# Kernel optimization log

Measured on AMD Instinct MI355X. Metric: run time of the kernel, lower is better.

## Reference

```python
import jax, jax.numpy as jnp
import numpy as np

NUM_HEADS = 16
HEAD_DIM = 128
D_MODEL = 2048
BATCH = 2
SEQ = 2048


def setup_inputs() -> dict:
    key = jax.random.key(0)
    ks = jax.random.split(key, 6)
    x = jax.random.normal(ks[0], (BATCH, SEQ, D_MODEL), dtype=jnp.float32)
    # RoPE tables (real/imag parts of freqs_cis), shape [S, HEAD_DIM//2]
    pos = jnp.arange(SEQ, dtype=jnp.float32)[:, None]
    inv_freq = 1.0 / (10000.0 ** (jnp.arange(0, HEAD_DIM, 2, dtype=jnp.float32) / HEAD_DIM))
    ang = pos * inv_freq[None, :]
    freq_cos = jnp.cos(ang)
    freq_sin = jnp.sin(ang)
    scale = 1.0 / np.sqrt(D_MODEL)
    wq = jax.random.normal(ks[1], (D_MODEL, NUM_HEADS * HEAD_DIM), dtype=jnp.float32) * scale
    wk = jax.random.normal(ks[2], (D_MODEL, NUM_HEADS * HEAD_DIM), dtype=jnp.float32) * scale
    wv = jax.random.normal(ks[3], (D_MODEL, NUM_HEADS * HEAD_DIM), dtype=jnp.float32) * scale
    wo = jax.random.normal(ks[4], (NUM_HEADS * HEAD_DIM, D_MODEL), dtype=jnp.float32) * scale
    return {"x": x, "freq_cos": freq_cos, "freq_sin": freq_sin,
            "wq": wq, "wk": wk, "wv": wv, "wo": wo}


def _rotate_half(t):
    half = t.shape[-1] // 2
    return jnp.concatenate([-t[..., half:], t[..., :half]], axis=-1)


def _apply_rope(q, k, freq_cos, freq_sin):
    # q, k: [B, H, S, D]; freq_cos/sin: [S_total, D//2]
    q = q.astype(jnp.float32)
    k = k.astype(jnp.float32)
    S = q.shape[2]
    cos = jnp.concatenate([freq_cos[:S], freq_cos[:S]], axis=-1)[None, None]  # [1,1,S,D]
    sin = jnp.concatenate([freq_sin[:S], freq_sin[:S]], axis=-1)[None, None]
    q_out = q * cos + _rotate_half(q) * sin
    k_out = k * cos + _rotate_half(k) * sin
    return q_out, k_out


def reference(x, freq_cos, freq_sin, wq, wk, wv, wo):
    B, S, D = x.shape
    H, hd = NUM_HEADS, HEAD_DIM
    q = (x @ wq).reshape(B, S, H, hd).transpose(0, 2, 1, 3)  # [B,H,S,hd]
    k = (x @ wk).reshape(B, S, H, hd).transpose(0, 2, 1, 3)
    v = (x @ wv).reshape(B, S, H, hd).transpose(0, 2, 1, 3)
    q, k = _apply_rope(q, k, freq_cos, freq_sin)
    # explicit causal attention (faithful to CPU/GPU path)
    logits = jnp.einsum('bhqd,bhkd->bhqk', q, k) / jnp.sqrt(jnp.float32(hd))
    mask = jnp.tril(jnp.ones((S, S), dtype=jnp.float32))
    logits = jnp.where(mask[None, None, :, :], logits, -1e10)
    weights = jax.nn.softmax(logits, axis=-1)
    out = jnp.einsum('bhqk,bhkd->bhqd', weights, v)  # [B,H,S,hd]
    out = out.transpose(0, 2, 1, 3).reshape(B, S, H * hd)
    return out @ wo
```

## Files before the change

kernel.cpp:

```cpp
#include <hip/hip_runtime.h>

typedef unsigned short u16;
typedef unsigned int u32;
typedef __attribute__((ext_vector_type(8))) short bf16x8;
typedef __attribute__((ext_vector_type(4))) short bf16x4;
typedef __attribute__((ext_vector_type(4))) float f32x4;
typedef __attribute__((ext_vector_type(16))) float f32x16;

#define MFMA(a, b, c) __builtin_amdgcn_mfma_f32_16x16x32_bf16(a, b, c, 0, 0, 0)
#define MFMA32(a, b, c) __builtin_amdgcn_mfma_f32_32x32x16_bf16(a, b, c, 0, 0, 0)
#define ASYNC16(g, l)                                                        \
  __builtin_amdgcn_global_load_lds(                                          \
      (const __attribute__((address_space(1))) u32*)(g),                     \
      (__attribute__((address_space(3))) u32*)(l), 16, 0, 0)

#define SBARRIER()                                                           \
  do {                                                                       \
    asm volatile("" ::: "memory");                                           \
    __builtin_amdgcn_s_barrier();                                            \
    asm volatile("" ::: "memory");                                           \
  } while (0)

__device__ __forceinline__ float b2f(u16 u) {
  union { u32 i; float f; } x; x.i = ((u32)u) << 16; return x.f;
}
__device__ __forceinline__ u16 f2b(float f) {
  union { float f; u32 i; } x; x.f = f;
  return (u16)((x.i + 0x7fff + ((x.i >> 16) & 1)) >> 16);
}
__device__ __forceinline__ f32x4 fzero4() { f32x4 z = {0.f, 0.f, 0.f, 0.f}; return z; }
__device__ __forceinline__ f32x16 fzero16() {
  f32x16 z;
#pragma unroll
  for (int i = 0; i < 16; ++i) z[i] = 0.f;
  return z;
}
__device__ __forceinline__ u32 pkbf16(float lo, float hi) {
  u32 r;
  asm("v_cvt_pk_bf16_f32 %0, %1, %2" : "=v"(r) : "v"(lo), "v"(hi));
  return r;
}

__global__ __launch_bounds__(256) void cvt_x(const float* __restrict__ src,
                                             u16* __restrict__ dst) {
  const int i = (blockIdx.x * 256 + threadIdx.x) * 4;
  const f32x4 v = *(const f32x4*)(src + i);
  bf16x4 o;
  o[0] = (short)f2b(v[0]); o[1] = (short)f2b(v[1]);
  o[2] = (short)f2b(v[2]); o[3] = (short)f2b(v[3]);
  *(bf16x4*)(dst + i) = o;
}

__global__ __launch_bounds__(256) void wtrans_f32(const float* __restrict__ src,
                                                  u16* __restrict__ dst) {
  __shared__ u16 tile[64][65];
  const int k0 = blockIdx.y * 64, n0 = blockIdx.x * 64;
  const int t = threadIdx.x;
  const int tr = t >> 3, tc = t & 7;

#pragma unroll
  for (int hh = 0; hh < 2; ++hh) {
    const int k = tr + hh * 32;
    const float* p = src + (size_t)(k0 + k) * 2048 + n0 + tc * 8;
    const f32x4 a = *(const f32x4*)(p);
    const f32x4 b = *(const f32x4*)(p + 4);
#pragma unroll
    for (int j = 0; j < 4; ++j) tile[k][tc * 8 + j] = f2b(a[j]);
#pragma unroll
    for (int j = 0; j < 4; ++j) tile[k][tc * 8 + 4 + j] = f2b(b[j]);
  }
  __syncthreads();
#pragma unroll
  for (int hh = 0; hh < 2; ++hh) {
    const int n = tr + hh * 32;
    bf16x8 v;
#pragma unroll
    for (int j = 0; j < 8; ++j) v[j] = (short)tile[tc * 8 + j][n];
    *(bf16x8*)(dst + (size_t)(n0 + n) * 2048 + k0 + tc * 8) = v;
  }
}

__global__ __launch_bounds__(256) void wtrans3(const float* __restrict__ wq,
                                               const float* __restrict__ wk,
                                               const float* __restrict__ wv,
                                               u16* __restrict__ wTall) {
  __shared__ u16 tile[64][65];
  const int z = blockIdx.z;
  const float* src = (z == 0) ? wq : (z == 1) ? wk : wv;
  u16* dst = wTall + (size_t)z * 2048 * 2048;
  const int k0 = blockIdx.y * 64, n0 = blockIdx.x * 64;
  const int t = threadIdx.x;
  const int tr = t >> 3, tc = t & 7;

#pragma unroll
  for (int hh = 0; hh < 2; ++hh) {
    const int k = tr + hh * 32;
    const float* p = src + (size_t)(k0 + k) * 2048 + n0 + tc * 8;
    const f32x4 a = *(const f32x4*)(p);
    const f32x4 b = *(const f32x4*)(p + 4);
#pragma unroll
    for (int j = 0; j < 4; ++j) tile[k][tc * 8 + j] = f2b(a[j]);
#pragma unroll
    for (int j = 0; j < 4; ++j) tile[k][tc * 8 + 4 + j] = f2b(b[j]);
  }
  __syncthreads();
#pragma unroll
  for (int hh = 0; hh < 2; ++hh) {
    const int n = tr + hh * 32;
    bf16x8 v;
#pragma unroll
    for (int j = 0; j < 8; ++j) v[j] = (short)tile[tc * 8 + j][n];
    *(bf16x8*)(dst + (size_t)(n0 + n) * 2048 + k0 + tc * 8) = v;
  }
}

__device__ __forceinline__ void gemm_mainloop(const u16* __restrict__ A,
                                              const u16* __restrict__ Bt,
                                              int K, int m0, int n0,
                                              u16* lA, u16* lB,
                                              f32x4 acc[4][4]) {
  const int tid = threadIdx.x;
  const int lane = tid & 63;
  const int wave = tid >> 6;
  const int quad = lane >> 4;
  const int l16 = lane & 15;
  const int wr = wave >> 1, wc = wave & 1;

  const int srow = lane >> 2;
  const int scol = (lane & 3) * 8;
  const u16* ga0 = A + (size_t)(m0 + (wave * 2 + 0) * 16 + srow) * K + scol;
  const u16* ga1 = A + (size_t)(m0 + (wave * 2 + 1) * 16 + srow) * K + scol;
  const u16* gb0 = Bt + (size_t)(n0 + (wave * 2 + 0) * 16 + srow) * K + scol;
  const u16* gb1 = Bt + (size_t)(n0 + (wave * 2 + 1) * 16 + srow) * K + scol;
  u16* la0 = lA + (wave * 2 + 0) * 512;
  u16* la1 = lA + (wave * 2 + 1) * 512;
  u16* lb0 = lB + (wave * 2 + 0) * 512;
  u16* lb1 = lB + (wave * 2 + 1) * 512;

  for (int k0 = 0; k0 < K; k0 += 32) {
    ASYNC16(ga0 + k0, la0);
    ASYNC16(ga1 + k0, la1);
    ASYNC16(gb0 + k0, lb0);
    ASYNC16(gb1 + k0, lb1);
    __syncthreads();
    bf16x8 af[4], bfr[4];
#pragma unroll
    for (int mb = 0; mb < 4; ++mb)
      af[mb] = *(const bf16x8*)(lA + ((wr * 64 + mb * 16 + l16) * 32 + quad * 8));
#pragma unroll
    for (int nb = 0; nb < 4; ++nb)
      bfr[nb] = *(const bf16x8*)(lB + ((wc * 64 + nb * 16 + l16) * 32 + quad * 8));
#pragma unroll
    for (int mb = 0; mb < 4; ++mb)
#pragma unroll
      for (int nb = 0; nb < 4; ++nb)
        acc[mb][nb] = MFMA(af[mb], bfr[nb], acc[mb][nb]);
    __syncthreads();
  }
}

__global__ __launch_bounds__(256) void gemm_qkv(const u16* __restrict__ x,
                                                const u16* __restrict__ wT,
                                                u16* __restrict__ qkv) {
  __shared__ u16 lA[128 * 32];
  __shared__ u16 lB[128 * 32];
  f32x4 acc[4][4];
#pragma unroll
  for (int i = 0; i < 4; ++i)
#pragma unroll
    for (int j = 0; j < 4; ++j) acc[i][j] = fzero4();

  const int m0 = blockIdx.y * 128, n0 = blockIdx.x * 128;
  gemm_mainloop(x, wT, 2048, m0, n0, lA, lB, acc);

  const int lane = threadIdx.x & 63, wave = threadIdx.x >> 6;
  const int quad = lane >> 4, l16 = lane & 15;
  const int wr = wave >> 1, wc = wave & 1;
#pragma unroll
  for (int mb = 0; mb < 4; ++mb)
#pragma unroll
    for (int nb = 0; nb < 4; ++nb)
#pragma unroll
      for (int r = 0; r < 4; ++r) {
        const int row = m0 + wr * 64 + mb * 16 + quad * 4 + r;
        const int col = n0 + wc * 64 + nb * 16 + l16;
        const int b = row >> 11, s = row & 2047;
        const int which = col >> 11, rem = col & 2047;
        const int hh = rem >> 7, d = rem & 127;
        const size_t idx = (size_t)which * ((size_t)4096 * 2048) +
                           (((size_t)(b * 16 + hh) * 2048 + s) * 128 + d);
        qkv[idx] = f2b(acc[mb][nb][r]);
      }
}

__global__ __launch_bounds__(512, 2) void gemm_out8(const u16* __restrict__ Oin,
                                                    const u16* __restrict__ woT,
                                                    float* __restrict__ out) {
  __shared__ u16 lds[3 * 24576];

  const int orig = blockIdx.x;
  const int wg = (orig & 7) * 32 + (orig >> 3);
  const int m0 = (wg >> 4) * 256;
  const int n0 = (wg & 15) * 128;

  const int tid = threadIdx.x;
  const int lane = tid & 63;
  const int wave = tid >> 6;
  const int quad = lane >> 4, l16 = lane & 15;
  const int wr = wave >> 2, wc = wave & 3;

  const int r0s = tid >> 3;
  const int c0s = (tid & 7) ^ (r0s & 7);
  const int r1s = r0s + 64;
  const int c1s = (tid & 7) ^ (r1s & 7);

  const u16* gA = Oin + (size_t)m0 * 2048;
  const u16* gB = woT + (size_t)n0 * 2048;

#define SLOT8(t) (lds + ((t) % 3) * 24576)
#define STAGE_A8(t)                                                          \
  do {                                                                       \
    u16* Lb0 = SLOT8(t) + wave * 512;                                        \
    const u16* g0 = gA + (t) * 64;                                           \
    ASYNC16(g0 + (size_t)r0s * 2048 + c0s * 8, Lb0);                         \
    ASYNC16(g0 + (size_t)r1s * 2048 + c1s * 8, Lb0 + 4096);                  \
    u16* Lb1 = SLOT8(t) + 8192 + wave * 512;                                 \
    const u16* g1 = gA + (size_t)128 * 2048 + (t) * 64;                      \
    ASYNC16(g1 + (size_t)r0s * 2048 + c0s * 8, Lb1);                         \
    ASYNC16(g1 + (size_t)r1s * 2048 + c1s * 8, Lb1 + 4096);                  \
  } while (0)
#define STAGE_B8(t)                                                          \
  do {                                                                       \
    u16* Lb = SLOT8(t) + 16384 + wave * 512;                                 \
    const u16* g = gB + (t) * 64;                                            \
    ASYNC16(g + (size_t)r0s * 2048 + c0s * 8, Lb);                           \
    ASYNC16(g + (size_t)r1s * 2048 + c1s * 8, Lb + 4096);                    \
  } while (0)

  f32x4 acc[8][2];
#pragma unroll
  for (int i = 0; i < 8; ++i) { acc[i][0] = fzero4(); acc[i][1] = fzero4(); }

  int aoff[8], boff[2];
#pragma unroll
  for (int mb = 0; mb < 8; ++mb) aoff[mb] = (wr * 128 + mb * 16 + l16) * 64;
#pragma unroll
  for (int nb = 0; nb < 2; ++nb) boff[nb] = 16384 + (wc * 32 + nb * 16 + l16) * 64;
  const int ach0 = ((0 * 4 + quad) ^ (l16 & 7)) * 8;
  const int ach1 = ((1 * 4 + quad) ^ (l16 & 7)) * 8;

  STAGE_A8(0); STAGE_B8(0);
  STAGE_A8(1); STAGE_B8(1);
  asm volatile("s_waitcnt vmcnt(6)" ::: "memory");
  SBARRIER();

  for (int t = 0; t < 32; ++t) {
    const u16* sl = SLOT8(t);
    bf16x8 af[8], bfr[2];

#pragma unroll
    for (int mb = 0; mb < 8; ++mb)
      af[mb] = *(const bf16x8*)(sl + aoff[mb] + ach0);
#pragma unroll
    for (int nb = 0; nb < 2; ++nb)
      bfr[nb] = *(const bf16x8*)(sl + boff[nb] + ach0);
    if (t < 30) STAGE_A8(t + 2);
    SBARRIER();
    asm volatile("s_waitcnt lgkmcnt(0)" ::: "memory");
    __builtin_amdgcn_s_setprio(1);
#pragma unroll
    for (int mb = 0; mb < 8; ++mb)
#pragma unroll
      for (int nb = 0; nb < 2; ++nb)
        acc[mb][nb] = MFMA(af[mb], bfr[nb], acc[mb][nb]);
    __builtin_amdgcn_s_setprio(0);
    SBARRIER();

#pragma unroll
    for (int mb = 0; mb < 8; ++mb)
      af[mb] = *(const bf16x8*)(sl + aoff[mb] + ach1);
#pragma unroll
    for (int nb = 0; nb < 2; ++nb)
      bfr[nb] = *(const bf16x8*)(sl + boff[nb] + ach1);
    if (t < 30) STAGE_B8(t + 2);
    SBARRIER();
    asm volatile("s_waitcnt lgkmcnt(0)" ::: "memory");
    __builtin_amdgcn_s_setprio(1);
#pragma unroll
    for (int mb = 0; mb < 8; ++mb)
#pragma unroll
      for (int nb = 0; nb < 2; ++nb)
        acc[mb][nb] = MFMA(af[mb], bfr[nb], acc[mb][nb]);
    __builtin_amdgcn_s_setprio(0);
    if (t <= 29) {
      asm volatile("s_waitcnt vmcnt(6)" ::: "memory");
    } else if (t == 30) {
      asm volatile("s_waitcnt vmcnt(0)" ::: "memory");
    }
    SBARRIER();
  }
#undef SLOT8
#undef STAGE_A8
#undef STAGE_B8

#pragma unroll
  for (int mb = 0; mb < 8; ++mb)
#pragma unroll
    for (int nb = 0; nb < 2; ++nb)
#pragma unroll
      for (int r = 0; r < 4; ++r) {
        const int row = m0 + wr * 128 + mb * 16 + quad * 4 + r;
        const int col = n0 + wc * 32 + nb * 16 + l16;
        out[(size_t)row * 2048 + col] = acc[mb][nb][r];
      }
}

__global__ __launch_bounds__(256) void rope_kernel(u16* __restrict__ Q,
                                                   u16* __restrict__ K,
                                                   const float* __restrict__ fcos,
                                                   const float* __restrict__ fsin) {
  const int i = blockIdx.x * 256 + threadIdx.x;
  const int d = i & 63;
  const int s = (i >> 6) & 2047;
  const int bh = i >> 17;
  const size_t base = ((size_t)bh * 2048 + s) * 128;
  const float c = fcos[s * 64 + d];
  const float sn = fsin[s * 64 + d];
  const float qs = 0.08838834764831845f;

  const float q0 = b2f(Q[base + d]), q1 = b2f(Q[base + d + 64]);
  Q[base + d] = f2b((q0 * c - q1 * sn) * qs);
  Q[base + d + 64] = f2b((q1 * c + q0 * sn) * qs);
  const float k0 = b2f(K[base + d]), k1 = b2f(K[base + d + 64]);
  K[base + d] = f2b(k0 * c - k1 * sn);
  K[base + d + 64] = f2b(k1 * c + k0 * sn);
}

template <int NB>
__device__ __forceinline__ void qkt_block(f32x16& sv, int n0, int qlo, int hi,
                                          int c, const u16* lK,
                                          const bf16x8* qf) {
  const int lo = n0 + NB * 32;
  if (lo < qlo + 32) {
    sv = fzero16();
    __builtin_amdgcn_s_setprio(1);
#pragma unroll
    for (int kc = 0; kc < 8; ++kc) {
      const bf16x8 kf =
          *(const bf16x8*)(lK + (NB * 32 + c) * 136 + kc * 16 + hi * 8);
      sv = MFMA32(kf, qf[kc], sv);
    }
    __builtin_amdgcn_s_setprio(0);
    if (lo == qlo) {
#pragma unroll
      for (int r = 0; r < 16; ++r) {
        const int n32 = (r & 3) + 8 * (r >> 2) + 4 * hi;
        if (n32 > c) sv[r] = -1e30f;
      }
    }
  } else {
#pragma unroll
    for (int r = 0; r < 16; ++r) sv[r] = -1e30f;
  }
}

template <int NB>
__device__ __forceinline__ void pv_block(const f32x16& sv, int n0, int qlo,
                                         int hi, int c, const u16* lV,
                                         f32x16* accO) {
  if (n0 + NB * 32 < qlo + 32) {
#pragma unroll
    for (int half = 0; half < 2; ++half) {
      const int rb = half * 8;
      const u32 pA = pkbf16(sv[rb + 0], sv[rb + 1]);
      const u32 pB = pkbf16(sv[rb + 2], sv[rb + 3]);
      const u32 pC = pkbf16(sv[rb + 4], sv[rb + 5]);
      const u32 pD = pkbf16(sv[rb + 6], sv[rb + 7]);
      const u32 xA = (u32)__shfl_xor((int)pA, 32);
      const u32 xB = (u32)__shfl_xor((int)pB, 32);
      const u32 xC = (u32)__shfl_xor((int)pC, 32);
      const u32 xD = (u32)__shfl_xor((int)pD, 32);
      bf16x8 pa;
      u32* pw = (u32*)&pa;
      pw[0] = hi ? xC : pA;
      pw[1] = hi ? xD : pB;
      pw[2] = hi ? pC : xA;
      pw[3] = hi ? pD : xB;
      __builtin_amdgcn_s_setprio(1);
#pragma unroll
      for (int db = 0; db < 4; ++db) {
        const bf16x8 vf = *(const bf16x8*)(lV + (db * 32 + c) * 72 +
                                           NB * 32 + half * 16 + hi * 8);
        accO[db] = MFMA32(pa, vf, accO[db]);
      }
      __builtin_amdgcn_s_setprio(0);
    }
  }
}

__global__ __launch_bounds__(256, 2) void attn4(const u16* __restrict__ Q,
                                                const u16* __restrict__ K,
                                                const u16* __restrict__ V,
                                                u16* __restrict__ O) {
  __shared__ u16 lK[64 * 136];
  __shared__ u16 lV[128 * 72];

  const int bid = blockIdx.x;
  const int bh = (bid & 7) + 8 * ((bid >> 3) & 3);
  const int tq = bid >> 5;
  const int qt = (tq < 8) ? tq : 23 - tq;
  const int q0 = qt * 128;
  const int b = bh >> 4, h = bh & 15;
  const u16* Qh = Q + (size_t)bh * 2048 * 128;
  const u16* Kh = K + (size_t)bh * 2048 * 128;
  const u16* Vh = V + (size_t)bh * 2048 * 128;

  const int tid = threadIdx.x;
  const int lane = tid & 63, wave = tid >> 6;
  const int hi = lane >> 5, c = lane & 31;
  const int qlo = q0 + wave * 32;
  const int krow = tid >> 4, kj = tid & 15;
  const int r0 = (tid & 31) * 2, d0v = (tid >> 5) * 16;

  bf16x8 qf[8];
  {
    const u16* qrow = Qh + (size_t)(q0 + wave * 32 + c) * 128 + hi * 8;
#pragma unroll
    for (int kc = 0; kc < 8; ++kc) qf[kc] = *(const bf16x8*)(qrow + kc * 16);
  }

  float m_i = -1e30f, l_i = 0.f;
  f32x16 accO[4];
#pragma unroll
  for (int db = 0; db < 4; ++db) accO[db] = fzero16();

  const int nIter = 2 * qt + 2;

  bf16x8 kreg[4], vreg[4];
  {
#pragma unroll
    for (int i = 0; i < 4; ++i)
      kreg[i] = *(const bf16x8*)(Kh + (size_t)(krow + 16 * i) * 128 + kj * 8);
    const u16* vp = Vh + (size_t)r0 * 128 + d0v;
    vreg[0] = *(const bf16x8*)(vp);
    vreg[1] = *(const bf16x8*)(vp + 8);
    vreg[2] = *(const bf16x8*)(vp + 128);
    vreg[3] = *(const bf16x8*)(vp + 136);
  }

  for (int it = 0; it < nIter; ++it) {
    const int n0 = it * 64;
#pragma unroll
    for (int i = 0; i < 4; ++i)
      *(bf16x8*)(lK + (krow + 16 * i) * 136 + kj * 8) = kreg[i];
#pragma unroll
    for (int j = 0; j < 8; ++j) {
      const u32 lo = (u16)vreg[0][j], hi2 = (u16)vreg[2][j];
      *(u32*)(lV + (d0v + j) * 72 + r0) = lo | (hi2 << 16);
    }
#pragma unroll
    for (int j = 0; j < 8; ++j) {
      const u32 lo = (u16)vreg[1][j], hi2 = (u16)vreg[3][j];
      *(u32*)(lV + (d0v + 8 + j) * 72 + r0) = lo | (hi2 << 16);
    }
    __syncthreads();

    if (it + 1 < nIter) {
      const int nn = n0 + 64;
#pragma unroll
      for (int i = 0; i < 4; ++i)
        kreg[i] =
            *(const bf16x8*)(Kh + (size_t)(nn + krow + 16 * i) * 128 + kj * 8);
      const u16* vp = Vh + (size_t)(nn + r0) * 128 + d0v;
      vreg[0] = *(const bf16x8*)(vp);
      vreg[1] = *(const bf16x8*)(vp + 8);
      vreg[2] = *(const bf16x8*)(vp + 128);
      vreg[3] = *(const bf16x8*)(vp + 136);
    }

    f32x16 s0, s1;
    qkt_block<0>(s0, n0, qlo, hi, c, lK, qf);
    qkt_block<1>(s1, n0, qlo, hi, c, lK, qf);

    float mx = -1e30f;
#pragma unroll
    for (int r = 0; r < 16; ++r) mx = fmaxf(mx, fmaxf(s0[r], s1[r]));
    mx = fmaxf(mx, __shfl_xor(mx, 32));
    if (!__all(mx - m_i <= 8.0f)) {
      const float mn = fmaxf(m_i, mx);
      const float alpha = __expf(m_i - mn);
      m_i = mn;
      l_i *= alpha;
#pragma unroll
      for (int r = 0; r < 16; ++r) {
        const int src = ((r & 3) + 8 * (r >> 2) + 4 * hi) + (lane & 32);
        const float aa = __shfl(alpha, src);
        accO[0][r] *= aa; accO[1][r] *= aa;
        accO[2][r] *= aa; accO[3][r] *= aa;
      }
    }
    float rs = 0.f;
#pragma unroll
    for (int r = 0; r < 16; ++r) {
      const float p0 = __expf(s0[r] - m_i);
      const float p1 = __expf(s1[r] - m_i);
      s0[r] = p0; s1[r] = p1;
      rs += p0 + p1;
    }
    rs += __shfl_xor(rs, 32);
    l_i += rs;

    pv_block<0>(s0, n0, qlo, hi, c, lV, accO);
    pv_block<1>(s1, n0, qlo, hi, c, lV, accO);
    __syncthreads();
  }

  const float linv = 1.f / l_i;
#pragma unroll
  for (int r = 0; r < 16; ++r) {
    const int q32 = (r & 3) + 8 * (r >> 2) + 4 * hi;
    const float inv = __shfl(linv, q32 + (lane & 32));
    const int srow = q0 + wave * 32 + q32;
    u16* orow = O + ((size_t)b * 2048 + srow) * 2048 + h * 128 + c;
#pragma unroll
    for (int db = 0; db < 4; ++db) orow[db * 32] = f2b(accO[db][r] * inv);
  }
}

extern "C" void kernel_launch(void* const* d_in, const int* in_sizes, int n_in,
                              void* d_out, int out_size, void* d_ws, size_t ws_size,
                              hipStream_t stream) {
  const float* x  = (const float*)d_in[0];
  const float* fc = (const float*)d_in[1];
  const float* fs = (const float*)d_in[2];
  const float* wq = (const float*)d_in[3];
  const float* wk = (const float*)d_in[4];
  const float* wv = (const float*)d_in[5];
  const float* wo = (const float*)d_in[6];
  float* out = (float*)d_out;

  u16* ws = (u16*)d_ws;
  const size_t BUF = (size_t)4096 * 2048;
  u16* xb  = ws;
  u16* Ob  = ws;
  u16* Qb  = ws + 1 * BUF;
  u16* Kb  = ws + 2 * BUF;
  u16* Vb  = ws + 3 * BUF;
  u16* wTall = (u16*)d_out;
  u16* woT = Kb;

  hipLaunchKernelGGL(cvt_x, dim3(8192), dim3(256), 0, stream, x, xb);
  hipLaunchKernelGGL(wtrans3, dim3(32, 32, 3), dim3(256), 0, stream, wq, wk, wv, wTall);
  hipLaunchKernelGGL(gemm_qkv, dim3(48, 32), dim3(256), 0, stream, xb, wTall, Qb);
  hipLaunchKernelGGL(rope_kernel, dim3(16384), dim3(256), 0, stream, Qb, Kb, fc, fs);
  hipLaunchKernelGGL(attn4, dim3(512), dim3(256), 0, stream, Qb, Kb, Vb, Ob);
  hipLaunchKernelGGL(wtrans_f32, dim3(32, 32), dim3(256), 0, stream, wo, woT);
  hipLaunchKernelGGL(gemm_out8, dim3(256), dim3(512), 0, stream, Ob, woT, out);
}
```

Before: 388.9 us.

## Replace QKV GEMM with triple-buffered 256x128 pipelined kernel from output projection

The simple QKV projection GEMM (128x128 tiles, single LDS buffer, two syncs per 32-wide k-step) is replaced by a copy of the tuned output-projection kernel. That kernel uses 256x128 tiles, 512 threads, a three-slot async LDS pipeline with XOR swizzle, and a remapped block order for cache locality. The epilogue keeps the head-major QKV scatter store. This aims to hide global load latency and raise MFMA utilisation, at the cost of more LDS per block and a fixed 768-block grid tied to these shapes.

```diff
diff --git a/kernel.cpp b/kernel.cpp
--- a/kernel.cpp
+++ b/kernel.cpp
@@ -114,94 +114,15 @@
   }
 }
 
-__device__ __forceinline__ void gemm_mainloop(const u16* __restrict__ A,
-                                              const u16* __restrict__ Bt,
-                                              int K, int m0, int n0,
-                                              u16* lA, u16* lB,
-                                              f32x4 acc[4][4]) {
-  const int tid = threadIdx.x;
-  const int lane = tid & 63;
-  const int wave = tid >> 6;
-  const int quad = lane >> 4;
-  const int l16 = lane & 15;
-  const int wr = wave >> 1, wc = wave & 1;
-
-  const int srow = lane >> 2;
-  const int scol = (lane & 3) * 8;
-  const u16* ga0 = A + (size_t)(m0 + (wave * 2 + 0) * 16 + srow) * K + scol;
-  const u16* ga1 = A + (size_t)(m0 + (wave * 2 + 1) * 16 + srow) * K + scol;
-  const u16* gb0 = Bt + (size_t)(n0 + (wave * 2 + 0) * 16 + srow) * K + scol;
-  const u16* gb1 = Bt + (size_t)(n0 + (wave * 2 + 1) * 16 + srow) * K + scol;
-  u16* la0 = lA + (wave * 2 + 0) * 512;
-  u16* la1 = lA + (wave * 2 + 1) * 512;
-  u16* lb0 = lB + (wave * 2 + 0) * 512;
-  u16* lb1 = lB + (wave * 2 + 1) * 512;
-
-  for (int k0 = 0; k0 < K; k0 += 32) {
-    ASYNC16(ga0 + k0, la0);
-    ASYNC16(ga1 + k0, la1);
-    ASYNC16(gb0 + k0, lb0);
-    ASYNC16(gb1 + k0, lb1);
-    __syncthreads();
-    bf16x8 af[4], bfr[4];
-#pragma unroll
-    for (int mb = 0; mb < 4; ++mb)
-      af[mb] = *(const bf16x8*)(lA + ((wr * 64 + mb * 16 + l16) * 32 + quad * 8));
-#pragma unroll
-    for (int nb = 0; nb < 4; ++nb)
-      bfr[nb] = *(const bf16x8*)(lB + ((wc * 64 + nb * 16 + l16) * 32 + quad * 8));
-#pragma unroll
-    for (int mb = 0; mb < 4; ++mb)
-#pragma unroll
-      for (int nb = 0; nb < 4; ++nb)
-        acc[mb][nb] = MFMA(af[mb], bfr[nb], acc[mb][nb]);
-    __syncthreads();
-  }
-}
-
-__global__ __launch_bounds__(256) void gemm_qkv(const u16* __restrict__ x,
-                                                const u16* __restrict__ wT,
-                                                u16* __restrict__ qkv) {
-  __shared__ u16 lA[128 * 32];
-  __shared__ u16 lB[128 * 32];
-  f32x4 acc[4][4];
-#pragma unroll
-  for (int i = 0; i < 4; ++i)
-#pragma unroll
-    for (int j = 0; j < 4; ++j) acc[i][j] = fzero4();
-
-  const int m0 = blockIdx.y * 128, n0 = blockIdx.x * 128;
-  gemm_mainloop(x, wT, 2048, m0, n0, lA, lB, acc);
-
-  const int lane = threadIdx.x & 63, wave = threadIdx.x >> 6;
-  const int quad = lane >> 4, l16 = lane & 15;
-  const int wr = wave >> 1, wc = wave & 1;
-#pragma unroll
-  for (int mb = 0; mb < 4; ++mb)
-#pragma unroll
-    for (int nb = 0; nb < 4; ++nb)
-#pragma unroll
-      for (int r = 0; r < 4; ++r) {
-        const int row = m0 + wr * 64 + mb * 16 + quad * 4 + r;
-        const int col = n0 + wc * 64 + nb * 16 + l16;
-        const int b = row >> 11, s = row & 2047;
-        const int which = col >> 11, rem = col & 2047;
-        const int hh = rem >> 7, d = rem & 127;
-        const size_t idx = (size_t)which * ((size_t)4096 * 2048) +
-                           (((size_t)(b * 16 + hh) * 2048 + s) * 128 + d);
-        qkv[idx] = f2b(acc[mb][nb][r]);
-      }
-}
-
-__global__ __launch_bounds__(512, 2) void gemm_out8(const u16* __restrict__ Oin,
-                                                    const u16* __restrict__ woT,
-                                                    float* __restrict__ out) {
+__global__ __launch_bounds__(512, 2) void gemm_qkv8(const u16* __restrict__ x,
+                                                    const u16* __restrict__ wT,
+                                                    u16* __restrict__ qkv) {
   __shared__ u16 lds[3 * 24576];
 
   const int orig = blockIdx.x;
-  const int wg = (orig & 7) * 32 + (orig >> 3);
-  const int m0 = (wg >> 4) * 256;
-  const int n0 = (wg & 15) * 128;
+  const int wg = (orig & 7) * 96 + (orig >> 3);
+  const int m0 = (wg & 15) * 256;
+  const int n0 = (wg >> 4) * 128;
 
   const int tid = threadIdx.x;
   const int lane = tid & 63;
@@ -214,8 +135,8 @@
   const int r1s = r0s + 64;
   const int c1s = (tid & 7) ^ (r1s & 7);
 
-  const u16* gA = Oin + (size_t)m0 * 2048;
-  const u16* gB = woT + (size_t)n0 * 2048;
+  const u16* gA = x + (size_t)m0 * 2048;
+  const u16* gB = wT + (size_t)n0 * 2048;
 
 #define SLOT8(t) (lds + ((t) % 3) * 24576)
 #define STAGE_A8(t)                                                          \
@@ -303,6 +224,134 @@
 #undef STAGE_A8
 #undef STAGE_B8
 
+  const size_t BUF = (size_t)4096 * 2048;
+#pragma unroll
+  for (int mb = 0; mb < 8; ++mb)
+#pragma unroll
+    for (int nb = 0; nb < 2; ++nb)
+#pragma unroll
+      for (int r = 0; r < 4; ++r) {
+        const int row = m0 + wr * 128 + mb * 16 + quad * 4 + r;
+        const int col = n0 + wc * 32 + nb * 16 + l16;
+        const int b = row >> 11, s = row & 2047;
+        const int which = col >> 11, rem = col & 2047;
+        const int hh = rem >> 7, d = rem & 127;
+        const size_t idx = (size_t)which * BUF +
+                           (((size_t)(b * 16 + hh) * 2048 + s) * 128 + d);
+        qkv[idx] = f2b(acc[mb][nb][r]);
+      }
+}
+
+__global__ __launch_bounds__(512, 2) void gemm_out8(const u16* __restrict__ Oin,
+                                                    const u16* __restrict__ woT,
+                                                    float* __restrict__ out) {
+  __shared__ u16 lds[3 * 24576];
+
+  const int orig = blockIdx.x;
+  const int wg = (orig & 7) * 32 + (orig >> 3);
+  const int m0 = (wg >> 4) * 256;
+  const int n0 = (wg & 15) * 128;
+
+  const int tid = threadIdx.x;
+  const int lane = tid & 63;
+  const int wave = tid >> 6;
+  const int quad = lane >> 4, l16 = lane & 15;
+  const int wr = wave >> 2, wc = wave & 3;
+
+  const int r0s = tid >> 3;
+  const int c0s = (tid & 7) ^ (r0s & 7);
+  const int r1s = r0s + 64;
+  const int c1s = (tid & 7) ^ (r1s & 7);
+
+  const u16* gA = Oin + (size_t)m0 * 2048;
+  const u16* gB = woT + (size_t)n0 * 2048;
+
+#define SLOT8(t) (lds + ((t) % 3) * 24576)
+#define STAGE_A8(t)                                                          \
+  do {                                                                       \
+    u16* Lb0 = SLOT8(t) + wave * 512;                                        \
+    const u16* g0 = gA + (t) * 64;                                           \
+    ASYNC16(g0 + (size_t)r0s * 2048 + c0s * 8, Lb0);                         \
+    ASYNC16(g0 + (size_t)r1s * 2048 + c1s * 8, Lb0 + 4096);                  \
+    u16* Lb1 = SLOT8(t) + 8192 + wave * 512;                                 \
+    const u16* g1 = gA + (size_t)128 * 2048 + (t) * 64;                      \
+    ASYNC16(g1 + (size_t)r0s * 2048 + c0s * 8, Lb1);                         \
+    ASYNC16(g1 + (size_t)r1s * 2048 + c1s * 8, Lb1 + 4096);                  \
+  } while (0)
+#define STAGE_B8(t)                                                          \
+  do {                                                                       \
+    u16* Lb = SLOT8(t) + 16384 + wave * 512;                                 \
+    const u16* g = gB + (t) * 64;                                            \
+    ASYNC16(g + (size_t)r0s * 2048 + c0s * 8, Lb);                           \
+    ASYNC16(g + (size_t)r1s * 2048 + c1s * 8, Lb + 4096);                    \
+  } while (0)
+
+  f32x4 acc[8][2];
+#pragma unroll
+  for (int i = 0; i < 8; ++i) { acc[i][0] = fzero4(); acc[i][1] = fzero4(); }
+
+  int aoff[8], boff[2];
+#pragma unroll
+  for (int mb = 0; mb < 8; ++mb) aoff[mb] = (wr * 128 + mb * 16 + l16) * 64;
+#pragma unroll
+  for (int nb = 0; nb < 2; ++nb) boff[nb] = 16384 + (wc * 32 + nb * 16 + l16) * 64;
+  const int ach0 = ((0 * 4 + quad) ^ (l16 & 7)) * 8;
+  const int ach1 = ((1 * 4 + quad) ^ (l16 & 7)) * 8;
+
+  STAGE_A8(0); STAGE_B8(0);
+  STAGE_A8(1); STAGE_B8(1);
+  asm volatile("s_waitcnt vmcnt(6)" ::: "memory");
+  SBARRIER();
+
+  for (int t = 0; t < 32; ++t) {
+    const u16* sl = SLOT8(t);
+    bf16x8 af[8], bfr[2];
+
+#pragma unroll
+    for (int mb = 0; mb < 8; ++mb)
+      af[mb] = *(const bf16x8*)(sl + aoff[mb] + ach0);
+#pragma unroll
+    for (int nb = 0; nb < 2; ++nb)
+      bfr[nb] = *(const bf16x8*)(sl + boff[nb] + ach0);
+    if (t < 30) STAGE_A8(t + 2);
+    SBARRIER();
+    asm volatile("s_waitcnt lgkmcnt(0)" ::: "memory");
+    __builtin_amdgcn_s_setprio(1);
+#pragma unroll
+    for (int mb = 0; mb < 8; ++mb)
+#pragma unroll
+      for (int nb = 0; nb < 2; ++nb)
+        acc[mb][nb] = MFMA(af[mb], bfr[nb], acc[mb][nb]);
+    __builtin_amdgcn_s_setprio(0);
+    SBARRIER();
+
+#pragma unroll
+    for (int mb = 0; mb < 8; ++mb)
+      af[mb] = *(const bf16x8*)(sl + aoff[mb] + ach1);
+#pragma unroll
+    for (int nb = 0; nb < 2; ++nb)
+      bfr[nb] = *(const bf16x8*)(sl + boff[nb] + ach1);
+    if (t < 30) STAGE_B8(t + 2);
+    SBARRIER();
+    asm volatile("s_waitcnt lgkmcnt(0)" ::: "memory");
+    __builtin_amdgcn_s_setprio(1);
+#pragma unroll
+    for (int mb = 0; mb < 8; ++mb)
+#pragma unroll
+      for (int nb = 0; nb < 2; ++nb)
+        acc[mb][nb] = MFMA(af[mb], bfr[nb], acc[mb][nb]);
+    __builtin_amdgcn_s_setprio(0);
+    if (t <= 29) {
+      asm volatile("s_waitcnt vmcnt(6)" ::: "memory");
+    } else if (t == 30) {
+      asm volatile("s_waitcnt vmcnt(0)" ::: "memory");
+    }
+    SBARRIER();
+  }
+#undef SLOT8
+#undef STAGE_A8
+#undef STAGE_B8
+
 #pragma unroll
   for (int mb = 0; mb < 8; ++mb)
 #pragma unroll
@@ -551,7 +600,7 @@
 
   hipLaunchKernelGGL(cvt_x, dim3(8192), dim3(256), 0, stream, x, xb);
   hipLaunchKernelGGL(wtrans3, dim3(32, 32, 3), dim3(256), 0, stream, wq, wk, wv, wTall);
-  hipLaunchKernelGGL(gemm_qkv, dim3(48, 32), dim3(256), 0, stream, xb, wTall, Qb);
+  hipLaunchKernelGGL(gemm_qkv8, dim3(768), dim3(512), 0, stream, xb, wTall, Qb);
   hipLaunchKernelGGL(rope_kernel, dim3(16384), dim3(256), 0, stream, Qb, Kb, fc, fs);
   hipLaunchKernelGGL(attn4, dim3(512), dim3(256), 0, stream, Qb, Kb, Vb, Ob);
   hipLaunchKernelGGL(wtrans_f32, dim3(32, 32), dim3(256), 0, stream, wo, woT);
```

New measurement: 378.6 us. 2.7% less time.

## Rewrite QKV GEMM with 256x256 tiles, triple-buffered async LDS pipeline, XCD-aware mapping

Applied to the files above, without the earlier changes.

Replaces the 128x128 single-buffered QKV projection GEMM with a 512-thread kernel computing 256x256 tiles. It uses a three-slot LDS ring filled by async global-to-LDS loads two steps ahead, split A/B staging interleaved with MFMA halves, and s_setprio around the MFMA bursts. Block indices are remapped so neighbouring tiles share an XCD for L2 reuse. The aim is to hide load latency and raise arithmetic intensity, at the cost of much higher register pressure (128 accumulator floats per lane) and hand-tuned waitcnt logic.

```diff
diff --git a/kernel.cpp b/kernel.cpp
--- a/kernel.cpp
+++ b/kernel.cpp
@@ -114,80 +114,120 @@
   }
 }
 
-__device__ __forceinline__ void gemm_mainloop(const u16* __restrict__ A,
-                                              const u16* __restrict__ Bt,
-                                              int K, int m0, int n0,
-                                              u16* lA, u16* lB,
-                                              f32x4 acc[4][4]) {
+__global__ __launch_bounds__(512, 2) void gemm_qkv9(const u16* __restrict__ x,
+                                                    const u16* __restrict__ wT,
+                                                    u16* __restrict__ qkv) {
+  __shared__ u16 lds[3 * 16384];
+
+  const int orig = blockIdx.x;
+  const int xcd = orig & 7, l = orig >> 3;
+  const int m0 = ((xcd >> 1) * 4 + (l & 3)) * 256;
+  const int n0 = ((xcd & 1) * 12 + (l >> 2)) * 256;
+
   const int tid = threadIdx.x;
   const int lane = tid & 63;
   const int wave = tid >> 6;
-  const int quad = lane >> 4;
-  const int l16 = lane & 15;
-  const int wr = wave >> 1, wc = wave & 1;
-
-  const int srow = lane >> 2;
-  const int scol = (lane & 3) * 8;
-  const u16* ga0 = A + (size_t)(m0 + (wave * 2 + 0) * 16 + srow) * K + scol;
-  const u16* ga1 = A + (size_t)(m0 + (wave * 2 + 1) * 16 + srow) * K + scol;
-  const u16* gb0 = Bt + (size_t)(n0 + (wave * 2 + 0) * 16 + srow) * K + scol;
-  const u16* gb1 = Bt + (size_t)(n0 + (wave * 2 + 1) * 16 + srow) * K + scol;
-  u16* la0 = lA + (wave * 2 + 0) * 512;
-  u16* la1 = lA + (wave * 2 + 1) * 512;
-  u16* lb0 = lB + (wave * 2 + 0) * 512;
-  u16* lb1 = lB + (wave * 2 + 1) * 512;
-
-  for (int k0 = 0; k0 < K; k0 += 32) {
-    ASYNC16(ga0 + k0, la0);
-    ASYNC16(ga1 + k0, la1);
-    ASYNC16(gb0 + k0, lb0);
-    ASYNC16(gb1 + k0, lb1);
-    __syncthreads();
+  const int quad = lane >> 4, l16 = lane & 15;
+  const int wr = wave >> 2, wc = wave & 3;
+
+  const int rs = tid & 255;
+  const int cs = tid >> 8;
+  const u16* gA = x + (size_t)(m0 + rs) * 2048 + cs * 8;
+  const u16* gB = wT + (size_t)(n0 + rs) * 2048 + cs * 8;
+  const int ldst = wave * 512;
+
+#define SLOT9(t) (lds + ((t) % 3) * 16384)
+#define STAGE_A9(t)                                                          \
+  do {                                                                       \
+    u16* d_ = SLOT9(t) + ldst;                                               \
+    ASYNC16(gA + (t) * 32, d_);                                              \
+    ASYNC16(gA + (t) * 32 + 16, d_ + 4096);                                  \
+  } while (0)
+#define STAGE_B9(t)                                                          \
+  do {                                                                       \
+    u16* d_ = SLOT9(t) + 8192 + ldst;                                        \
+    ASYNC16(gB + (t) * 32, d_);                                              \
+    ASYNC16(gB + (t) * 32 + 16, d_ + 4096);                                  \
+  } while (0)
+
+  f32x4 acc[8][4];
+#pragma unroll
+  for (int i = 0; i < 8; ++i)
+#pragma unroll
+    for (int j = 0; j < 4; ++j) acc[i][j] = fzero4();
+
+  int aoff[8], boff[4];
+#pragma unroll
+  for (int mb = 0; mb < 8; ++mb)
+    aoff[mb] = quad * 2048 + (wr * 128 + mb * 16 + l16) * 8;
+#pragma unroll
+  for (int nb = 0; nb < 4; ++nb)
+    boff[nb] = 8192 + quad * 2048 + (wc * 64 + nb * 16 + l16) * 8;
+
+  STAGE_A9(0); STAGE_B9(0);
+  STAGE_A9(1); STAGE_B9(1);
+  asm volatile("s_waitcnt vmcnt(4)" ::: "memory");
+  SBARRIER();
+
+  for (int t = 0; t < 64; ++t) {
+    const u16* sl = SLOT9(t);
     bf16x8 af[4], bfr[4];
+
 #pragma unroll
     for (int mb = 0; mb < 4; ++mb)
-      af[mb] = *(const bf16x8*)(lA + ((wr * 64 + mb * 16 + l16) * 32 + quad * 8));
+      af[mb] = *(const bf16x8*)(sl + aoff[mb]);
 #pragma unroll
     for (int nb = 0; nb < 4; ++nb)
-      bfr[nb] = *(const bf16x8*)(lB + ((wc * 64 + nb * 16 + l16) * 32 + quad * 8));
+      bfr[nb] = *(const bf16x8*)(sl + boff[nb]);
+    if (t < 62) STAGE_A9(t + 2);
+    SBARRIER();
+    asm volatile("s_waitcnt lgkmcnt(0)" ::: "memory");
+    __builtin_amdgcn_s_setprio(1);
 #pragma unroll
     for (int mb = 0; mb < 4; ++mb)
 #pragma unroll
       for (int nb = 0; nb < 4; ++nb)
         acc[mb][nb] = MFMA(af[mb], bfr[nb], acc[mb][nb]);
-    __syncthreads();
-  }
-}
-
-__global__ __launch_bounds__(256) void gemm_qkv(const u16* __restrict__ x,
-                                                const u16* __restrict__ wT,
-                                                u16* __restrict__ qkv) {
-  __shared__ u16 lA[128 * 32];
-  __shared__ u16 lB[128 * 32];
-  f32x4 acc[4][4];
-#pragma unroll
-  for (int i = 0; i < 4; ++i)
-#pragma unroll
-    for (int j = 0; j < 4; ++j) acc[i][j] = fzero4();
-
-  const int m0 = blockIdx.y * 128, n0 = blockIdx.x * 128;
-  gemm_mainloop(x, wT, 2048, m0, n0, lA, lB, acc);
-
-  const int lane = threadIdx.x & 63, wave = threadIdx.x >> 6;
-  const int quad = lane >> 4, l16 = lane & 15;
-  const int wr = wave >> 1, wc = wave & 1;
-#pragma unroll
-  for (int mb = 0; mb < 4; ++mb)
+    __builtin_amdgcn_s_setprio(0);
+    SBARRIER();
+
+#pragma unroll
+    for (int mb = 0; mb < 4; ++mb)
+      af[mb] = *(const bf16x8*)(sl + aoff[mb + 4]);
+    if (t < 62) STAGE_B9(t + 2);
+    SBARRIER();
+    asm volatile("s_waitcnt lgkmcnt(0)" ::: "memory");
+    __builtin_amdgcn_s_setprio(1);
+#pragma unroll
+    for (int mb = 0; mb < 4; ++mb)
+#pragma unroll
+      for (int nb = 0; nb < 4; ++nb)
+        acc[mb + 4][nb] = MFMA(af[mb], bfr[nb], acc[mb + 4][nb]);
+    __builtin_amdgcn_s_setprio(0);
+    if (t <= 61) {
+      asm volatile("s_waitcnt vmcnt(4)" ::: "memory");
+    } else if (t == 62) {
+      asm volatile("s_waitcnt vmcnt(0)" ::: "memory");
+    }
+    SBARRIER();
+  }
+#undef SLOT9
+#undef STAGE_A9
+#undef STAGE_B9
+
+  const size_t BUF = (size_t)4096 * 2048;
+#pragma unroll
+  for (int mb = 0; mb < 8; ++mb)
 #pragma unroll
     for (int nb = 0; nb < 4; ++nb)
 #pragma unroll
       for (int r = 0; r < 4; ++r) {
-        const int row = m0 + wr * 64 + mb * 16 + quad * 4 + r;
+        const int row = m0 + wr * 128 + mb * 16 + quad * 4 + r;
         const int col = n0 + wc * 64 + nb * 16 + l16;
         const int b = row >> 11, s = row & 2047;
         const int which = col >> 11, rem = col & 2047;
         const int hh = rem >> 7, d = rem & 127;
-        const size_t idx = (size_t)which * ((size_t)4096 * 2048) +
+        const size_t idx = (size_t)which * BUF +
                            (((size_t)(b * 16 + hh) * 2048 + s) * 128 + d);
         qkv[idx] = f2b(acc[mb][nb][r]);
       }
@@ -551,7 +591,7 @@
 
   hipLaunchKernelGGL(cvt_x, dim3(8192), dim3(256), 0, stream, x, xb);
   hipLaunchKernelGGL(wtrans3, dim3(32, 32, 3), dim3(256), 0, stream, wq, wk, wv, wTall);
-  hipLaunchKernelGGL(gemm_qkv, dim3(48, 32), dim3(256), 0, stream, xb, wTall, Qb);
+  hipLaunchKernelGGL(gemm_qkv9, dim3(384), dim3(512), 0, stream, xb, wTall, Qb);
   hipLaunchKernelGGL(rope_kernel, dim3(16384), dim3(256), 0, stream, Qb, Kb, fc, fs);
   hipLaunchKernelGGL(attn4, dim3(512), dim3(256), 0, stream, Qb, Kb, Vb, Ob);
   hipLaunchKernelGGL(wtrans_f32, dim3(32, 32), dim3(256), 0, stream, wo, woT);
```

After: 423.2 us. 8.8% more time.
